# Kernel optimization log

Measured on AMD Instinct MI355X. Metric: run time of the kernel, lower is better.

Reference implementation:

```python
import jax, jax.numpy as jnp
import numpy as np

N_NODES = 200000
N_EDGES = 3200000
F_IN = 16
N_CLASSES = 16


def setup_inputs() -> dict:
    key = jax.random.key(0)
    ks = jax.random.split(key, 8)
    s = 1.0 / np.sqrt(F_IN)
    return {
        "x": jax.random.normal(ks[0], (N_NODES, F_IN), dtype=jnp.float32),
        "edge_index": jax.random.randint(ks[1], (2, N_EDGES), 0, N_NODES, dtype=jnp.int32),
        "eps1": jnp.zeros((), dtype=jnp.float32),
        "w1a": jax.random.normal(ks[2], (F_IN, 16), dtype=jnp.float32) * s,
        "b1a": jnp.zeros((16,), dtype=jnp.float32),
        "w1b": jax.random.normal(ks[3], (16, 16), dtype=jnp.float32) * 0.25,
        "b1b": jnp.zeros((16,), dtype=jnp.float32),
        "eps2": jnp.zeros((), dtype=jnp.float32),
        "w2a": jax.random.normal(ks[4], (16, N_CLASSES), dtype=jnp.float32) * 0.25,
        "b2a": jnp.zeros((N_CLASSES,), dtype=jnp.float32),
        "w2b": jax.random.normal(ks[5], (N_CLASSES, N_CLASSES), dtype=jnp.float32) * 0.25,
        "b2b": jnp.zeros((N_CLASSES,), dtype=jnp.float32),
    }


def _gin_conv(x, src, dst, eps, wa, ba, wb, bb, n_nodes):
    # sum aggregation of source-node features into destination nodes
    agg = jax.ops.segment_sum(x[src], dst, num_segments=n_nodes)  # [N, F]
    h = (1.0 + eps) * x + agg
    # 2-layer MLP: Linear -> ReLU -> Linear
    h = jax.nn.relu(h @ wa + ba) @ wb + bb
    return h


def reference(x, edge_index, eps1, w1a, b1a, w1b, b1b, eps2, w2a, b2a, w2b, b2b):
    src, dst = edge_index[0], edge_index[1]
    n = x.shape[0]
    h = jax.nn.relu(_gin_conv(x, src, dst, eps1, w1a, b1a, w1b, b1b, n))
    # F.dropout with training=False is identity (module assumed in eval mode)
    h = _gin_conv(h, src, dst, eps2, w2a, b2a, w2b, b2b, n)
    return jax.nn.log_softmax(h, axis=1)
```

## Files before the change

### kernel.cpp

```cpp
#include <hip/hip_runtime.h>

#define N_NODES 200000
#define N_EDGES 3200000
#define F 16
#define NB 782
#define NB_PAD 832
#define EPB 16384
#define EBLOCKS ((N_EDGES + EPB - 1) / EPB)
#define ET 1024
#define CAP 5120
#define SORT_T 512
#define SPLIT 100000
#define GIN_NODES 64
#define GIN_BLOCKS ((N_NODES + GIN_NODES - 1) / GIN_NODES)


typedef int iv4 __attribute__((ext_vector_type(4)));

__device__ __forceinline__ int ntload(const int* p) {
    return __builtin_nontemporal_load(p);
}
__device__ __forceinline__ iv4 ntload4(const int* p) {
    return __builtin_nontemporal_load((const iv4*)p);
}

__device__ __forceinline__ unsigned bf16pack2(float lo, float hi) {
    unsigned ul = __float_as_uint(lo);
    unsigned uh = __float_as_uint(hi);
    ul = (ul + 0x7fffu + ((ul >> 16) & 1u)) >> 16;
    uh = (uh + 0x7fffu + ((uh >> 16) & 1u)) >> 16;
    return ul | (uh << 16);
}
#define BLO(w) __uint_as_float((w) << 16)
#define BHI(w) __uint_as_float((w) & 0xffff0000u)

__device__ __forceinline__ void acc8(uint4 w0, uint4 w1, float acc[16]) {
    acc[0]  += BLO(w0.x); acc[1]  += BHI(w0.x);
    acc[2]  += BLO(w0.y); acc[3]  += BHI(w0.y);
    acc[4]  += BLO(w0.z); acc[5]  += BHI(w0.z);
    acc[6]  += BLO(w0.w); acc[7]  += BHI(w0.w);
    acc[8]  += BLO(w1.x); acc[9]  += BHI(w1.x);
    acc[10] += BLO(w1.y); acc[11] += BHI(w1.y);
    acc[12] += BLO(w1.z); acc[13] += BHI(w1.z);
    acc[14] += BLO(w1.w); acc[15] += BHI(w1.w);
}

__device__ __forceinline__ void gather_range(
    const unsigned short* __restrict__ xin,
    const int* __restrict__ ebuf,
    int lo, int hi, int sub, float acc[16]) {
    int k = lo + sub;
    for (; k + 12 < hi; k += 16) {
        int s0 = ntload(ebuf + k);
        int s1 = ntload(ebuf + k + 4);
        int s2 = ntload(ebuf + k + 8);
        int s3 = ntload(ebuf + k + 12);
        const uint4* r0 = (const uint4*)(xin + (size_t)s0 * F);
        const uint4* r1 = (const uint4*)(xin + (size_t)s1 * F);
        const uint4* r2 = (const uint4*)(xin + (size_t)s2 * F);
        const uint4* r3 = (const uint4*)(xin + (size_t)s3 * F);
        uint4 a0 = r0[0], a1 = r0[1];
        uint4 b0 = r1[0], b1 = r1[1];
        uint4 c0 = r2[0], c1 = r2[1];
        uint4 d0 = r3[0], d1 = r3[1];
        acc8(a0, a1, acc); acc8(b0, b1, acc);
        acc8(c0, c1, acc); acc8(d0, d1, acc);
    }
    for (; k + 4 < hi; k += 8) {
        int s0 = ntload(ebuf + k);
        int s1 = ntload(ebuf + k + 4);
        const uint4* r0 = (const uint4*)(xin + (size_t)s0 * F);
        const uint4* r1 = (const uint4*)(xin + (size_t)s1 * F);
        uint4 a0 = r0[0], a1 = r0[1];
        uint4 b0 = r1[0], b1 = r1[1];
        acc8(a0, a1, acc); acc8(b0, b1, acc);
    }
    if (k < hi) {
        const uint4* r0 = (const uint4*)(xin + (size_t)ntload(ebuf + k) * F);
        acc8(r0[0], r0[1], acc);
    }
}


__global__ __launch_bounds__(256) void conv_bf16(const float* __restrict__ x,
                                                 unsigned* __restrict__ xb) {
    int i = blockIdx.x * blockDim.x + threadIdx.x;
    if (i >= N_NODES * F / 8) return;
    const float4* p = (const float4*)(x + (size_t)i * 8);
    float4 a = p[0], b = p[1];
    uint4 r;
    r.x = bf16pack2(a.x, a.y);
    r.y = bf16pack2(a.z, a.w);
    r.z = bf16pack2(b.x, b.y);
    r.w = bf16pack2(b.z, b.w);
    ((uint4*)xb)[i] = r;
}


__global__ __launch_bounds__(ET) void count_kernel(const int* __restrict__ dst,
                                                   int* __restrict__ cntmat) {
    __shared__ int lh[NB];
    const int t = threadIdx.x;
    for (int i = t; i < NB; i += ET) lh[i] = 0;
    __syncthreads();

    const int base4 = blockIdx.x * (EPB / 4);
    #pragma unroll
    for (int k = 0; k < EPB / 4 / ET; ++k) {
        int i4 = base4 + k * ET + t;
        if (i4 < N_EDGES / 4) {
            iv4 d = ntload4(dst + i4 * 4);
            atomicAdd(&lh[d.x >> 8], 1);
            atomicAdd(&lh[d.y >> 8], 1);
            atomicAdd(&lh[d.z >> 8], 1);
            atomicAdd(&lh[d.w >> 8], 1);
        }
    }
    __syncthreads();
    int* row = cntmat + (size_t)blockIdx.x * NB_PAD;
    for (int i = t; i < NB; i += ET) row[i] = lh[i];
}


__global__ __launch_bounds__(512) void colscan(int* __restrict__ cntmat,
                                               int* __restrict__ bcnt) {
    __shared__ int part[512];
    const int t = threadIdx.x;
    const int b = blockIdx.x;
    int v = 0;
    if (t < EBLOCKS) v = cntmat[(size_t)t * NB_PAD + b];
    part[t] = v;
    __syncthreads();
    for (int off = 1; off < 512; off <<= 1) {
        int o = (t >= off) ? part[t - off] : 0;
        __syncthreads();
        part[t] += o;
        __syncthreads();
    }
    if (t < EBLOCKS) cntmat[(size_t)t * NB_PAD + b] = part[t] - v;
    if (t == EBLOCKS - 1) bcnt[b] = part[t];
}


__global__ __launch_bounds__(1024) void bucket_scan(const int* __restrict__ bcnt,
                                                    int* __restrict__ bbase) {
    __shared__ int part[1024];
    const int t = threadIdx.x;
    int v = (t < NB) ? bcnt[t] : 0;
    part[t] = v;
    __syncthreads();
    for (int off = 1; off < 1024; off <<= 1) {
        int other = (t >= off) ? part[t - off] : 0;
        __syncthreads();
        part[t] += other;
        __syncthreads();
    }
    if (t < NB) bbase[t] = part[t] - v;
    if (t == 1023) bbase[NB] = part[1023];
}


__global__ __launch_bounds__(ET) void partition2(const int* __restrict__ src,
                                                 const int* __restrict__ dst,
                                                 const int* __restrict__ bbase,
                                                 const int* __restrict__ cntmat,
                                                 int* __restrict__ ebuf) {
    __shared__ int lh[NB];
    __shared__ int sbase[NB];
    const int t = threadIdx.x;
    const int* row = cntmat + (size_t)blockIdx.x * NB_PAD;
    for (int i = t; i < NB; i += ET) {
        sbase[i] = bbase[i] + row[i];
        lh[i] = 0;
    }
    __syncthreads();

    const int base4 = blockIdx.x * (EPB / 4);
    #pragma unroll
    for (int k = 0; k < EPB / 4 / ET; ++k) {
        int i4 = base4 + k * ET + t;
        if (i4 < N_EDGES / 4) {
            iv4 s = ntload4(src + i4 * 4);
            iv4 d = ntload4(dst + i4 * 4);
            int b, p;
            b = d.x >> 8; p = atomicAdd(&lh[b], 1); ebuf[sbase[b] + p] = (s.x << 8) | (d.x & 255);
            b = d.y >> 8; p = atomicAdd(&lh[b], 1); ebuf[sbase[b] + p] = (s.y << 8) | (d.y & 255);
            b = d.z >> 8; p = atomicAdd(&lh[b], 1); ebuf[sbase[b] + p] = (s.z << 8) | (d.z & 255);
            b = d.w >> 8; p = atomicAdd(&lh[b], 1); ebuf[sbase[b] + p] = (s.w << 8) | (d.w & 255);
        }
    }
}


__global__ __launch_bounds__(SORT_T) void sort_csr(const int* __restrict__ bbase,
                                                   int* __restrict__ ebuf,
                                                   int* __restrict__ noffs,
                                                   int* __restrict__ nmid,
                                                   int* __restrict__ scratch) {
    __shared__ int srec[CAP];
    __shared__ int hist[512];
    __shared__ int lofs[512];
    const int t = threadIdx.x;
    const int b = blockIdx.x;
    hist[t] = 0;
    __syncthreads();

    const int beg = bbase[b];
    const int end = bbase[b + 1];
    const int sz = end - beg;

    for (int k = beg + t; k < end; k += SORT_T) {
        int rec = ntload(ebuf + k);
        int bin = ((rec & 255) << 1) | ((rec >> 8) >= SPLIT);
        atomicAdd(&hist[bin], 1);
    }
    __syncthreads();
    int v = hist[t];
    lofs[t] = v;
    __syncthreads();
    for (int off = 1; off < 512; off <<= 1) {
        int o = (t >= off) ? lofs[t - off] : 0;
        __syncthreads();
        lofs[t] += o;
        __syncthreads();
    }
    const int myend = lofs[t];
    const int mybeg = myend - v;
    __syncthreads();
    hist[t] = mybeg;
    __syncthreads();

    if (sz <= CAP) {
        for (int k = beg + t; k < end; k += SORT_T) {
            int rec = ntload(ebuf + k);
            int bin = ((rec & 255) << 1) | ((rec >> 8) >= SPLIT);
            int p = atomicAdd(&hist[bin], 1);
            srec[p] = rec >> 8;
        }
        __syncthreads();
        for (int k = t; k < sz; k += SORT_T) ebuf[beg + k] = srec[k];
    } else {
        for (int k = beg + t; k < end; k += SORT_T) scratch[k] = ebuf[k];
        __syncthreads();
        for (int k = beg + t; k < end; k += SORT_T) {
            int rec = scratch[k];
            int bin = ((rec & 255) << 1) | ((rec >> 8) >= SPLIT);
            int p = atomicAdd(&hist[bin], 1);
            ebuf[beg + p] = rec >> 8;
        }
    }

    const int n = b * 256 + (t >> 1);
    if (n < N_NODES) {
        if ((t & 1) == 0) noffs[n] = beg + mybeg;
        else              nmid[n]  = beg + mybeg;
    }
    if (b == 0 && t == 0) noffs[N_NODES] = N_EDGES;
}


template <bool LAYER2>
__global__ __launch_bounds__(256) void gin_gather(
    const unsigned short* __restrict__ xin,
    const int* __restrict__ noffs,
    const int* __restrict__ nmid,
    const int* __restrict__ ebuf,
    const float* __restrict__ epsp,
    const float* __restrict__ wa, const float* __restrict__ ba,
    const float* __restrict__ wb, const float* __restrict__ bb,
    void* __restrict__ outp) {
    __shared__ float swa[256], swb[256], sba[16], sbb[16];
    const int t = threadIdx.x;
    swa[t] = wa[t];
    swb[t] = wb[t];
    if (t < 16) { sba[t] = ba[t]; sbb[t] = bb[t]; }
    __syncthreads();

    const int n = blockIdx.x * GIN_NODES + (t >> 2);
    const int sub = t & 3;
    if (n >= N_NODES) return;

    const int beg = noffs[n];
    const int mid = nmid[n];
    const int end = noffs[n + 1];

    float acc[16];
    #pragma unroll
    for (int q = 0; q < 16; ++q) acc[q] = 0.0f;

    gather_range(xin, ebuf, beg, mid, sub, acc);
    gather_range(xin, ebuf, mid, end, sub, acc);

    #pragma unroll
    for (int q = 0; q < 16; ++q) {
        acc[q] += __shfl_xor(acc[q], 1);
        acc[q] += __shfl_xor(acc[q], 2);
    }
    if (sub != 0) return;

    const float eps = 1.0f + *epsp;
    const uint4* xr = (const uint4*)(xin + (size_t)n * F);
    uint4 w0 = xr[0], w1 = xr[1];
    float h[16];
    h[0]  = fmaf(eps, BLO(w0.x), acc[0]);   h[1]  = fmaf(eps, BHI(w0.x), acc[1]);
    h[2]  = fmaf(eps, BLO(w0.y), acc[2]);   h[3]  = fmaf(eps, BHI(w0.y), acc[3]);
    h[4]  = fmaf(eps, BLO(w0.z), acc[4]);   h[5]  = fmaf(eps, BHI(w0.z), acc[5]);
    h[6]  = fmaf(eps, BLO(w0.w), acc[6]);   h[7]  = fmaf(eps, BHI(w0.w), acc[7]);
    h[8]  = fmaf(eps, BLO(w1.x), acc[8]);   h[9]  = fmaf(eps, BHI(w1.x), acc[9]);
    h[10] = fmaf(eps, BLO(w1.y), acc[10]);  h[11] = fmaf(eps, BHI(w1.y), acc[11]);
    h[12] = fmaf(eps, BLO(w1.z), acc[12]);  h[13] = fmaf(eps, BHI(w1.z), acc[13]);
    h[14] = fmaf(eps, BLO(w1.w), acc[14]);  h[15] = fmaf(eps, BHI(w1.w), acc[15]);

    float m[16];
    #pragma unroll
    for (int jj = 0; jj < 16; ++jj) {
        float a = sba[jj];
        #pragma unroll
        for (int i = 0; i < 16; ++i) a = fmaf(h[i], swa[i * 16 + jj], a);
        m[jj] = fmaxf(a, 0.0f);
    }

    float o[16];
    #pragma unroll
    for (int jj = 0; jj < 16; ++jj) {
        float a = sbb[jj];
        #pragma unroll
        for (int i = 0; i < 16; ++i) a = fmaf(m[i], swb[i * 16 + jj], a);
        o[jj] = LAYER2 ? a : fmaxf(a, 0.0f);
    }

    if (LAYER2) {
        float mx = o[0];
        #pragma unroll
        for (int jj = 1; jj < 16; ++jj) mx = fmaxf(mx, o[jj]);
        float s = 0.0f;
        #pragma unroll
        for (int jj = 0; jj < 16; ++jj) s += expf(o[jj] - mx);
        float lse = mx + logf(s);
        float* orow = (float*)outp + (size_t)n * F;
        #pragma unroll
        for (int q = 0; q < 4; ++q) {
            ((float4*)orow)[q] = make_float4(o[q * 4 + 0] - lse, o[q * 4 + 1] - lse,
                                             o[q * 4 + 2] - lse, o[q * 4 + 3] - lse);
        }
    } else {
        unsigned* orow = (unsigned*)outp + (size_t)n * 8;
        uint4 r0, r1;
        r0.x = bf16pack2(o[0],  o[1]);   r0.y = bf16pack2(o[2],  o[3]);
        r0.z = bf16pack2(o[4],  o[5]);   r0.w = bf16pack2(o[6],  o[7]);
        r1.x = bf16pack2(o[8],  o[9]);   r1.y = bf16pack2(o[10], o[11]);
        r1.z = bf16pack2(o[12], o[13]);  r1.w = bf16pack2(o[14], o[15]);
        ((uint4*)orow)[0] = r0;
        ((uint4*)orow)[1] = r1;
    }
}


__global__ __launch_bounds__(256) void scatter_kernel(
    const float* __restrict__ feat,
    const int* __restrict__ src,
    const int* __restrict__ dst,
    float* __restrict__ agg) {
    int e = blockIdx.x * blockDim.x + threadIdx.x;
    if (e >= N_EDGES) return;
    int s = src[e];
    int d = dst[e];
    const float4* fs = (const float4*)(feat + (size_t)s * F);
    float* ad = agg + (size_t)d * F;
    #pragma unroll
    for (int q = 0; q < 4; ++q) {
        float4 v = fs[q];
        atomicAdd(ad + q * 4 + 0, v.x);
        atomicAdd(ad + q * 4 + 1, v.y);
        atomicAdd(ad + q * 4 + 2, v.z);
        atomicAdd(ad + q * 4 + 3, v.w);
    }
}

template <bool RELU_OUT, bool LOGSOFTMAX>
__global__ __launch_bounds__(256) void mlp_kernel(
    const float* __restrict__ xin,
    const float* __restrict__ agg,
    const float* __restrict__ epsp,
    const float* __restrict__ wa, const float* __restrict__ ba,
    const float* __restrict__ wb, const float* __restrict__ bb,
    float* __restrict__ out) {
    __shared__ float swa[256], swb[256], sba[16], sbb[16];
    int t = threadIdx.x;
    swa[t] = wa[t];
    swb[t] = wb[t];
    if (t < 16) { sba[t] = ba[t]; sbb[t] = bb[t]; }
    __syncthreads();

    int n = blockIdx.x * blockDim.x + t;
    if (n >= N_NODES) return;

    float eps = 1.0f + *epsp;
    const float4* xr = (const float4*)(xin + (size_t)n * F);
    const float4* ar = (const float4*)(agg + (size_t)n * F);
    float h[16];
    #pragma unroll
    for (int q = 0; q < 4; ++q) {
        float4 xv = xr[q];
        float4 av = ar[q];
        h[q * 4 + 0] = fmaf(eps, xv.x, av.x);
        h[q * 4 + 1] = fmaf(eps, xv.y, av.y);
        h[q * 4 + 2] = fmaf(eps, xv.z, av.z);
        h[q * 4 + 3] = fmaf(eps, xv.w, av.w);
    }

    float m[16];
    #pragma unroll
    for (int jj = 0; jj < 16; ++jj) {
        float a = sba[jj];
        #pragma unroll
        for (int i = 0; i < 16; ++i) a = fmaf(h[i], swa[i * 16 + jj], a);
        m[jj] = fmaxf(a, 0.0f);
    }

    float o[16];
    #pragma unroll
    for (int jj = 0; jj < 16; ++jj) {
        float a = sbb[jj];
        #pragma unroll
        for (int i = 0; i < 16; ++i) a = fmaf(m[i], swb[i * 16 + jj], a);
        o[jj] = RELU_OUT ? fmaxf(a, 0.0f) : a;
    }

    if (LOGSOFTMAX) {
        float mx = o[0];
        #pragma unroll
        for (int jj = 1; jj < 16; ++jj) mx = fmaxf(mx, o[jj]);
        float s = 0.0f;
        #pragma unroll
        for (int jj = 0; jj < 16; ++jj) s += expf(o[jj] - mx);
        float lse = mx + logf(s);
        #pragma unroll
        for (int jj = 0; jj < 16; ++jj) o[jj] -= lse;
    }

    float4* orow = (float4*)(out + (size_t)n * F);
    #pragma unroll
    for (int q = 0; q < 4; ++q) {
        orow[q] = make_float4(o[q * 4 + 0], o[q * 4 + 1], o[q * 4 + 2], o[q * 4 + 3]);
    }
}


extern "C" void kernel_launch(void* const* d_in, const int* in_sizes, int n_in,
                              void* d_out, int out_size, void* d_ws, size_t ws_size,
                              hipStream_t stream) {
    const float* x    = (const float*)d_in[0];
    const int*   ei   = (const int*)d_in[1];
    const float* eps1 = (const float*)d_in[2];
    const float* w1a  = (const float*)d_in[3];
    const float* b1a  = (const float*)d_in[4];
    const float* w1b  = (const float*)d_in[5];
    const float* b1b  = (const float*)d_in[6];
    const float* eps2 = (const float*)d_in[7];
    const float* w2a  = (const float*)d_in[8];
    const float* b2a  = (const float*)d_in[9];
    const float* w2b  = (const float*)d_in[10];
    const float* b2b  = (const float*)d_in[11];

    float* out = (float*)d_out;
    const int* src = ei;
    const int* dst = ei + N_EDGES;

    size_t off_bcnt   = 0;
    size_t off_bbase  = off_bcnt + (size_t)NB_PAD * 4;
    size_t off_noffs  = off_bbase + (size_t)NB_PAD * 4;
    size_t off_nmid   = off_noffs + ((size_t)N_NODES + 64) * 4;
    size_t off_ebuf   = off_nmid + ((size_t)N_NODES + 64) * 4;
    size_t off_xb     = off_ebuf + (size_t)N_EDGES * 4;
    size_t off_hb     = off_xb + (size_t)N_NODES * F * 2;
    size_t off_cnt    = off_hb + (size_t)N_NODES * F * 2;
    size_t need       = off_cnt + (size_t)EBLOCKS * NB_PAD * 4;

    if (ws_size >= need) {
        int*            bcnt   = (int*)((char*)d_ws + off_bcnt);
        int*            bbase  = (int*)((char*)d_ws + off_bbase);
        int*            noffs  = (int*)((char*)d_ws + off_noffs);
        int*            nmid   = (int*)((char*)d_ws + off_nmid);
        int*            ebuf   = (int*)((char*)d_ws + off_ebuf);
        unsigned short* xb     = (unsigned short*)((char*)d_ws + off_xb);
        unsigned short* hb     = (unsigned short*)((char*)d_ws + off_hb);
        int*            cntmat = (int*)((char*)d_ws + off_cnt);

        count_kernel<<<EBLOCKS, ET, 0, stream>>>(dst, cntmat);
        conv_bf16<<<(N_NODES * F / 8 + 255) / 256, 256, 0, stream>>>(x, (unsigned*)xb);
        colscan<<<NB, 512, 0, stream>>>(cntmat, bcnt);
        bucket_scan<<<1, 1024, 0, stream>>>(bcnt, bbase);
        partition2<<<EBLOCKS, ET, 0, stream>>>(src, dst, bbase, cntmat, ebuf);
        sort_csr<<<NB, SORT_T, 0, stream>>>(bbase, ebuf, noffs, nmid, (int*)d_out);

        gin_gather<false><<<GIN_BLOCKS, 256, 0, stream>>>(
            xb, noffs, nmid, ebuf, eps1, w1a, b1a, w1b, b1b, hb);
        gin_gather<true><<<GIN_BLOCKS, 256, 0, stream>>>(
            hb, noffs, nmid, ebuf, eps2, w2a, b2a, w2b, b2b, out);
    } else {
        float* agg = (float*)d_ws;
        const int edge_blocks = (N_EDGES + 255) / 256;
        const int node_blocks = (N_NODES + 255) / 256;
        const size_t agg_bytes = (size_t)N_NODES * F * sizeof(float);

        hipMemsetAsync(agg, 0, agg_bytes, stream);
        scatter_kernel<<<edge_blocks, 256, 0, stream>>>(x, src, dst, agg);
        mlp_kernel<true, false><<<node_blocks, 256, 0, stream>>>(
            x, agg, eps1, w1a, b1a, w1b, b1b, out);

        hipMemsetAsync(agg, 0, agg_bytes, stream);
        scatter_kernel<<<edge_blocks, 256, 0, stream>>>(out, src, dst, agg);
        mlp_kernel<false, true><<<node_blocks, 256, 0, stream>>>(
            out, agg, eps2, w2a, b2a, w2b, b2b, out);
    }
}
```

Before: 178.6 us.

## Split GIN gather into two source-half passes and halve edges per block

Each GIN layer's gather is split into two kernels. The first sums neighbours whose source index is in the lower half of the nodes and stores fp32 partials in the output buffer. The second sums the upper half, adds the partials and runs the MLP. The goal is to keep each pass's randomly gathered feature working set small enough to stay in cache. It also halves edges per block in the count and partition kernels and replaces nontemporal loads with ordinary loads. In exchange it adds two launches and an extra fp32 write and read of partials per layer.

Result: no change. 179.2 us (+0.4%).

```diff
diff --git a/kernel.cpp b/kernel.cpp
--- a/kernel.cpp
+++ b/kernel.cpp
@@ -5,7 +5,7 @@
 #define F 16
 #define NB 782
 #define NB_PAD 832
-#define EPB 16384
+#define EPB 8192
 #define EBLOCKS ((N_EDGES + EPB - 1) / EPB)
 #define ET 1024
 #define CAP 5120
@@ -15,13 +15,11 @@
 #define GIN_BLOCKS ((N_NODES + GIN_NODES - 1) / GIN_NODES)
 
 
-typedef int iv4 __attribute__((ext_vector_type(4)));
+typedef int   iv4 __attribute__((ext_vector_type(4)));
+typedef float fv4 __attribute__((ext_vector_type(4)));
 
 __device__ __forceinline__ int ntload(const int* p) {
     return __builtin_nontemporal_load(p);
-}
-__device__ __forceinline__ iv4 ntload4(const int* p) {
-    return __builtin_nontemporal_load((const iv4*)p);
 }
 
 __device__ __forceinline__ unsigned bf16pack2(float lo, float hi) {
@@ -109,7 +107,7 @@
     for (int k = 0; k < EPB / 4 / ET; ++k) {
         int i4 = base4 + k * ET + t;
         if (i4 < N_EDGES / 4) {
-            iv4 d = ntload4(dst + i4 * 4);
+            int4 d = *(const int4*)(dst + i4 * 4);
             atomicAdd(&lh[d.x >> 8], 1);
             atomicAdd(&lh[d.y >> 8], 1);
             atomicAdd(&lh[d.z >> 8], 1);
@@ -180,8 +178,8 @@
     for (int k = 0; k < EPB / 4 / ET; ++k) {
         int i4 = base4 + k * ET + t;
         if (i4 < N_EDGES / 4) {
-            iv4 s = ntload4(src + i4 * 4);
-            iv4 d = ntload4(dst + i4 * 4);
+            int4 s = *(const int4*)(src + i4 * 4);
+            int4 d = *(const int4*)(dst + i4 * 4);
             int b, p;
             b = d.x >> 8; p = atomicAdd(&lh[b], 1); ebuf[sbase[b] + p] = (s.x << 8) | (d.x & 255);
             b = d.y >> 8; p = atomicAdd(&lh[b], 1); ebuf[sbase[b] + p] = (s.y << 8) | (d.y & 255);
@@ -210,7 +208,7 @@
     const int sz = end - beg;
 
     for (int k = beg + t; k < end; k += SORT_T) {
-        int rec = ntload(ebuf + k);
+        int rec = ebuf[k];
         int bin = ((rec & 255) << 1) | ((rec >> 8) >= SPLIT);
         atomicAdd(&hist[bin], 1);
     }
@@ -232,7 +230,7 @@
 
     if (sz <= CAP) {
         for (int k = beg + t; k < end; k += SORT_T) {
-            int rec = ntload(ebuf + k);
+            int rec = ebuf[k];
             int bin = ((rec & 255) << 1) | ((rec >> 8) >= SPLIT);
             int p = atomicAdd(&hist[bin], 1);
             srec[p] = rec >> 8;
@@ -259,12 +257,49 @@
 }
 
 
-template <bool LAYER2>
-__global__ __launch_bounds__(256) void gin_gather(
+__global__ __launch_bounds__(256) void gin_phaseA(
     const unsigned short* __restrict__ xin,
     const int* __restrict__ noffs,
     const int* __restrict__ nmid,
     const int* __restrict__ ebuf,
+    float* __restrict__ accb) {
+    const int t = threadIdx.x;
+    const int n = blockIdx.x * GIN_NODES + (t >> 2);
+    const int sub = t & 3;
+    if (n >= N_NODES) return;
+
+    const int beg = noffs[n];
+    const int mid = nmid[n];
+
+    float acc[16];
+    #pragma unroll
+    for (int q = 0; q < 16; ++q) acc[q] = 0.0f;
+
+    gather_range(xin, ebuf, beg, mid, sub, acc);
+
+    #pragma unroll
+    for (int q = 0; q < 16; ++q) {
+        acc[q] += __shfl_xor(acc[q], 1);
+        acc[q] += __shfl_xor(acc[q], 2);
+    }
+    if (sub != 0) return;
+
+    fv4* row = (fv4*)(accb + (size_t)n * F);
+    #pragma unroll
+    for (int q = 0; q < 4; ++q) {
+        fv4 v = {acc[q * 4 + 0], acc[q * 4 + 1], acc[q * 4 + 2], acc[q * 4 + 3]};
+        __builtin_nontemporal_store(v, row + q);
+    }
+}
+
+
+template <bool LAYER2>
+__global__ __launch_bounds__(256) void gin_phaseB(
+    const unsigned short* __restrict__ xin,
+    const int* __restrict__ noffs,
+    const int* __restrict__ nmid,
+    const int* __restrict__ ebuf,
+    const float* __restrict__ accb,
     const float* __restrict__ epsp,
     const float* __restrict__ wa, const float* __restrict__ ba,
     const float* __restrict__ wb, const float* __restrict__ bb,
@@ -280,7 +315,6 @@
     const int sub = t & 3;
     if (n >= N_NODES) return;
 
-    const int beg = noffs[n];
     const int mid = nmid[n];
     const int end = noffs[n + 1];
 
@@ -288,7 +322,6 @@
     #pragma unroll
     for (int q = 0; q < 16; ++q) acc[q] = 0.0f;
 
-    gather_range(xin, ebuf, beg, mid, sub, acc);
     gather_range(xin, ebuf, mid, end, sub, acc);
 
     #pragma unroll
@@ -297,6 +330,16 @@
         acc[q] += __shfl_xor(acc[q], 2);
     }
     if (sub != 0) return;
+
+    const fv4* arow = (const fv4*)(accb + (size_t)n * F);
+    #pragma unroll
+    for (int q = 0; q < 4; ++q) {
+        fv4 v = __builtin_nontemporal_load(arow + q);
+        acc[q * 4 + 0] += v.x;
+        acc[q * 4 + 1] += v.y;
+        acc[q * 4 + 2] += v.z;
+        acc[q * 4 + 3] += v.w;
+    }
 
     const float eps = 1.0f + *epsp;
     const uint4* xr = (const uint4*)(xin + (size_t)n * F);
@@ -486,6 +529,7 @@
         unsigned short* xb     = (unsigned short*)((char*)d_ws + off_xb);
         unsigned short* hb     = (unsigned short*)((char*)d_ws + off_hb);
         int*            cntmat = (int*)((char*)d_ws + off_cnt);
+        float*          accb   = (float*)d_out;
 
         count_kernel<<<EBLOCKS, ET, 0, stream>>>(dst, cntmat);
         conv_bf16<<<(N_NODES * F / 8 + 255) / 256, 256, 0, stream>>>(x, (unsigned*)xb);
@@ -494,10 +538,12 @@
         partition2<<<EBLOCKS, ET, 0, stream>>>(src, dst, bbase, cntmat, ebuf);
         sort_csr<<<NB, SORT_T, 0, stream>>>(bbase, ebuf, noffs, nmid, (int*)d_out);
 
-        gin_gather<false><<<GIN_BLOCKS, 256, 0, stream>>>(
-            xb, noffs, nmid, ebuf, eps1, w1a, b1a, w1b, b1b, hb);
-        gin_gather<true><<<GIN_BLOCKS, 256, 0, stream>>>(
-            hb, noffs, nmid, ebuf, eps2, w2a, b2a, w2b, b2b, out);
+        gin_phaseA<<<GIN_BLOCKS, 256, 0, stream>>>(xb, noffs, nmid, ebuf, accb);
+        gin_phaseB<false><<<GIN_BLOCKS, 256, 0, stream>>>(
+            xb, noffs, nmid, ebuf, accb, eps1, w1a, b1a, w1b, b1b, hb);
+        gin_phaseA<<<GIN_BLOCKS, 256, 0, stream>>>(hb, noffs, nmid, ebuf, accb);
+        gin_phaseB<true><<<GIN_BLOCKS, 256, 0, stream>>>(
+            hb, noffs, nmid, ebuf, accb, eps2, w2a, b2a, w2b, b2b, out);
     } else {
         float* agg = (float*)d_ws;
         const int edge_blocks = (N_EDGES + 255) / 256;
```
